# Optimization experiments

Hardware: AMD Instinct MI355X
Metric: run time of the kernel (lower is better)

The kernel has to match this reference:

```python
import jax, jax.numpy as jnp
import numpy as np

D_IN, HID = 128, 256
N_A, N_T = 120000, 30000
E_AT, E_TA, E_AA = 2_000_000, 2_000_000, 3_000_000
OUTS = [("artist", 129), ("style", 32), ("genre", 18)]


def setup_inputs() -> dict:
    key = jax.random.key(0)
    ks = jax.random.split(key, 32)

    def w(k, shape, fan_in):
        return jax.random.normal(k, shape, jnp.float32) / np.float32(np.sqrt(fan_in))

    def edges(k, e, n_src, n_dst):
        k1, k2 = jax.random.split(k)
        return jnp.stack([jax.random.randint(k1, (e,), 0, n_src),
                          jax.random.randint(k2, (e,), 0, n_dst)]).astype(jnp.int32)

    inp = {}
    inp["x_artwork"] = jax.random.normal(ks[0], (N_A, D_IN), jnp.float32)
    inp["x_tag"] = jax.random.normal(ks[1], (N_T, D_IN), jnp.float32)
    inp["edge_at"] = edges(ks[2], E_AT, N_A, N_T)
    inp["edge_ta"] = edges(ks[3], E_TA, N_T, N_A)
    inp["edge_aa"] = edges(ks[4], E_AA, N_A, N_A)
    # layer-1 weights shared shape across 3 gnns (G) and 3 relations (R): [G,R,din,H]
    inp["Wl1"] = w(ks[5], (3, 3, D_IN, HID), D_IN)
    inp["Wr1"] = w(ks[6], (3, 3, D_IN, HID), D_IN)
    inp["b1"] = jnp.zeros((3, 3, HID), jnp.float32)
    for i, (name, o) in enumerate(OUTS):
        inp[f"Wl2_{name}"] = w(ks[7 + 3 * i], (3, HID, o), HID)
        inp[f"Wr2_{name}"] = w(ks[8 + 3 * i], (3, HID, o), HID)
        inp[f"b2_{name}"] = jnp.zeros((3, o), jnp.float32)
    return inp


def _seg_mean(feat, dst, n):
    # PyG mean aggregation: sum over in-edges / count, 0 for isolated nodes
    s = jax.ops.segment_sum(feat, dst, num_segments=n)
    c = jax.ops.segment_sum(jnp.ones((dst.shape[0], 1), feat.dtype), dst, num_segments=n)
    return s / jnp.maximum(c, 1.0)


def _hetero_sage(xa, xt, e_at, e_ta, e_aa, Wl, Wr, b):
    # Wl/Wr: [3, din, dout] (rel order: at, ta, aa), b: [3, dout]
    m_at = _seg_mean(xa[e_at[0]], e_at[1], xt.shape[0])
    h_t = m_at @ Wl[0] + b[0] + xt @ Wr[0]
    m_ta = _seg_mean(xt[e_ta[0]], e_ta[1], xa.shape[0])
    m_aa = _seg_mean(xa[e_aa[0]], e_aa[1], xa.shape[0])
    h_a = (m_ta @ Wl[1] + b[1] + xa @ Wr[1]) + (m_aa @ Wl[2] + b[2] + xa @ Wr[2])
    return h_a, h_t


def _dropout(x, key, rate=0.5):
    keep = jax.random.bernoulli(key, 1.0 - rate, x.shape)
    return jnp.where(keep, x / (1.0 - rate), jnp.zeros((), x.dtype))


def _gnn(g, xa, xt, e_at, e_ta, e_aa, Wl1, Wr1, b1, Wl2, Wr2, b2):
    h_a, h_t = _hetero_sage(xa, xt, e_at, e_ta, e_aa, Wl1, Wr1, b1)
    h_a, h_t = jax.nn.relu(h_a), jax.nn.relu(h_t)
    k1, k2 = jax.random.split(jax.random.fold_in(jax.random.key(42), g))
    h_a, h_t = _dropout(h_a, k1), _dropout(h_t, k2)
    o_a, o_t = _hetero_sage(h_a, h_t, e_at, e_ta, e_aa, Wl2, Wr2, b2)
    return jax.nn.log_softmax(o_a, axis=1), jax.nn.log_softmax(o_t, axis=1)


def reference(x_artwork, x_tag, edge_at, edge_ta, edge_aa, Wl1, Wr1, b1,
              Wl2_artist, Wr2_artist, b2_artist,
              Wl2_style, Wr2_style, b2_style,
              Wl2_genre, Wr2_genre, b2_genre):
    l2 = [(Wl2_artist, Wr2_artist, b2_artist),
          (Wl2_style, Wr2_style, b2_style),
          (Wl2_genre, Wr2_genre, b2_genre)]
    outs = []
    for g in range(3):
        Wl2, Wr2, b2 = l2[g]
        o_a, o_t = _gnn(g, x_artwork, x_tag, edge_at, edge_ta, edge_aa,
                        Wl1[g], Wr1[g], b1[g], Wl2, Wr2, b2)
        outs.extend([o_a, o_t])
    return tuple(outs)
```

## Files before the change

### kernel.cpp

```cpp
#include <hip/hip_runtime.h>
#include <stdint.h>
#include <stddef.h>

typedef unsigned short bf16;
typedef __attribute__((ext_vector_type(8))) short short8;
typedef __attribute__((ext_vector_type(4))) float f32x4;

__device__ __forceinline__ float bf2f(unsigned short u){
  union { uint32_t i; float f; } x; x.i = ((uint32_t)u) << 16; return x.f;
}
__device__ __forceinline__ unsigned short f2bf(float f){
  union { float f; uint32_t i; } x; x.f = f;
  uint32_t r = x.i + 0x7FFFu + ((x.i >> 16) & 1u);
  return (unsigned short)(r >> 16);
}
__device__ __forceinline__ uint32_t pk2(float a, float b){
  return (uint32_t)f2bf(a) | ((uint32_t)f2bf(b) << 16);
}

__device__ __forceinline__ uint8_t f2fp8(float f){
  uint32_t b = __float_as_uint(f);
  uint32_t s = (b >> 24) & 0x80u;
  uint32_t x = b & 0x7fffffffu;
  if (x >= 0x43e00000u) return (uint8_t)(s | 0x7eu);
  if (x < 0x3c800000u){
    uint32_t q = (uint32_t)rintf(__uint_as_float(x) * 512.f);
    return (uint8_t)(s | q);
  }
  uint32_t lsb = (x >> 20) & 1u;
  x += 0x7ffffu + lsb;
  uint32_t u = (((x >> 23) - 120u) << 3) | ((x >> 20) & 7u);
  if (u > 0x7eu) u = 0x7eu;
  return (uint8_t)(s | u);
}
__device__ __forceinline__ float fp8d(uint8_t u){
  uint32_t e = (u >> 3) & 15u, m = u & 7u;
  float v = (e == 0) ? (float)m * 0.001953125f
                     : ldexpf((float)(8u + m), (int)e - 10);
  return (u & 0x80u) ? -v : v;
}

__host__ __device__ __forceinline__ uint32_t rotl32_(uint32_t x, int d){
  return (x << d) | (x >> (32 - d));
}
__host__ __device__ inline void tf2x32(uint32_t k0, uint32_t k1, uint32_t x0, uint32_t x1,
                                       uint32_t* o0, uint32_t* o1){
  uint32_t k2 = k0 ^ k1 ^ 0x1BD11BDAu;
#define TF_R4(ra,rb,rc,rd) \
  x0 += x1; x1 = rotl32_(x1,ra); x1 ^= x0; \
  x0 += x1; x1 = rotl32_(x1,rb); x1 ^= x0; \
  x0 += x1; x1 = rotl32_(x1,rc); x1 ^= x0; \
  x0 += x1; x1 = rotl32_(x1,rd); x1 ^= x0;
  x0 += k0; x1 += k1;
  TF_R4(13,15,26,6)  x0 += k1; x1 += k2 + 1u;
  TF_R4(17,29,16,24) x0 += k2; x1 += k0 + 2u;
  TF_R4(13,15,26,6)  x0 += k0; x1 += k1 + 3u;
  TF_R4(17,29,16,24) x0 += k1; x1 += k2 + 4u;
  TF_R4(13,15,26,6)  x0 += k2; x1 += k0 + 5u;
  *o0 = x0; *o1 = x1;
#undef TF_R4
}

__global__ void k_zeroi(int* __restrict__ p, int n){
  int i = blockIdx.x * 256 + threadIdx.x;
  if (i < n) p[i] = 0;
}
__global__ void k_f2bf(const float* __restrict__ in, bf16* __restrict__ out, int n4){
  int i = blockIdx.x * 256 + threadIdx.x;
  if (i < n4){
    float4 v = ((const float4*)in)[i];
    ushort4 u; u.x = f2bf(v.x); u.y = f2bf(v.y); u.z = f2bf(v.z); u.w = f2bf(v.w);
    ((ushort4*)out)[i] = u;
  }
}

__global__ void k_deg(const int* __restrict__ dst, int* __restrict__ deg, int E){
  int i = blockIdx.x * 256 + threadIdx.x;
  if (i < E) atomicAdd(&deg[dst[i]], 1);
}
__global__ __launch_bounds__(256)
void k_scan_partial(const int* __restrict__ in, int* __restrict__ exc,
                    int* __restrict__ bsum, int n){
  __shared__ int tmp[256];
  int t = threadIdx.x, i = blockIdx.x * 256 + t;
  int v = (i < n) ? in[i] : 0;
  tmp[t] = v; __syncthreads();
  #pragma unroll
  for (int off = 1; off < 256; off <<= 1){
    int u = (t >= off) ? tmp[t - off] : 0; __syncthreads();
    tmp[t] += u; __syncthreads();
  }
  if (i < n) exc[i] = tmp[t] - v;
  if (t == 255) bsum[blockIdx.x] = tmp[255];
}
__global__ __launch_bounds__(1024)
void k_scan_bsum(int* __restrict__ bsum, int nb, int* __restrict__ total_out){
  __shared__ int tmp[1024];
  int t = threadIdx.x;
  int v = (t < nb) ? bsum[t] : 0;
  tmp[t] = v; __syncthreads();
  #pragma unroll
  for (int off = 1; off < 1024; off <<= 1){
    int u = (t >= off) ? tmp[t - off] : 0; __syncthreads();
    tmp[t] += u; __syncthreads();
  }
  if (t < nb) bsum[t] = tmp[t] - v;
  if (t == 1023) *total_out = tmp[1023];
}
__global__ void k_scan_add(int* __restrict__ exc, const int* __restrict__ bsum, int n){
  int i = blockIdx.x * 256 + threadIdx.x;
  if (i < n) exc[i] += bsum[blockIdx.x];
}
__global__ void k_fill(const int* __restrict__ src, const int* __restrict__ dst,
                       const int* __restrict__ rs, int* __restrict__ cur,
                       int* __restrict__ cs, int E){
  int i = blockIdx.x * 256 + threadIdx.x;
  if (i < E){
    int d = dst[i];
    int p = atomicAdd(&cur[d], 1);
    cs[rs[d] + p] = src[i];
  }
}

__global__ __launch_bounds__(64)
void k_agg128b(const bf16* __restrict__ X, const int* __restrict__ rs,
               const int* __restrict__ cs, bf16* __restrict__ out){
  int node = blockIdx.x, lane = threadIdx.x;
  int s0 = rs[node], s1 = rs[node + 1];
  float ax = 0.f, ay = 0.f;
  int e = s0;
  for (; e + 4 <= s1; e += 4){
    int c0 = cs[e], c1 = cs[e+1], c2 = cs[e+2], c3 = cs[e+3];
    uint32_t v0 = ((const uint32_t*)(X + (size_t)c0 * 128))[lane];
    uint32_t v1 = ((const uint32_t*)(X + (size_t)c1 * 128))[lane];
    uint32_t v2 = ((const uint32_t*)(X + (size_t)c2 * 128))[lane];
    uint32_t v3 = ((const uint32_t*)(X + (size_t)c3 * 128))[lane];
    ax += bf2f((unsigned short)(v0 & 0xffffu)) + bf2f((unsigned short)(v1 & 0xffffu))
        + bf2f((unsigned short)(v2 & 0xffffu)) + bf2f((unsigned short)(v3 & 0xffffu));
    ay += bf2f((unsigned short)(v0 >> 16)) + bf2f((unsigned short)(v1 >> 16))
        + bf2f((unsigned short)(v2 >> 16)) + bf2f((unsigned short)(v3 >> 16));
  }
  for (; e < s1; ++e){
    uint32_t v = ((const uint32_t*)(X + (size_t)cs[e] * 128))[lane];
    ax += bf2f((unsigned short)(v & 0xffffu));
    ay += bf2f((unsigned short)(v >> 16));
  }
  float inv = 1.f / fmaxf((float)(s1 - s0), 1.f);
  ((uint32_t*)(out + (size_t)node * 128))[lane] = pk2(ax * inv, ay * inv);
}

__global__ void k_wt1a(const float* __restrict__ Wl1g, const float* __restrict__ Wr1g,
                       bf16* __restrict__ dst){
  int n = blockIdx.y, k = blockIdx.x * 128 + threadIdx.x;
  int seg = k >> 7, kk = k & 127;
  float v;
  if (seg == 0)      v = Wl1g[(size_t)(128 + kk) * 256 + n];
  else if (seg == 1) v = Wl1g[(size_t)(256 + kk) * 256 + n];
  else               v = Wr1g[(size_t)(128 + kk) * 256 + n] + Wr1g[(size_t)(256 + kk) * 256 + n];
  dst[(size_t)n * 384 + k] = f2bf(v);
}
__global__ void k_wt1t(const float* __restrict__ Wl1g, const float* __restrict__ Wr1g,
                       bf16* __restrict__ dst){
  int n = blockIdx.y, k = blockIdx.x * 128 + threadIdx.x;
  int kk = k & 127;
  float v = (k < 128) ? Wl1g[(size_t)kk * 256 + n] : Wr1g[(size_t)kk * 256 + n];
  dst[(size_t)n * 256 + k] = f2bf(v);
}
__global__ void k_wt2a(const float* __restrict__ Wl2g, const float* __restrict__ Wr2g,
                       int O, bf16* __restrict__ dst){
  int n = blockIdx.y, k = blockIdx.x * 128 + threadIdx.x;
  int strip = n / O, r = n - strip * O;
  float v;
  if (strip == 0)      v = Wl2g[(size_t)k * O + r];
  else if (strip == 1) v = Wl2g[(size_t)512 * O + (size_t)k * O + r];
  else                 v = Wr2g[(size_t)256 * O + (size_t)k * O + r]
                         + Wr2g[(size_t)512 * O + (size_t)k * O + r];
  dst[(size_t)n * 256 + k] = f2bf(v);
}
__global__ void k_wt2t(const float* __restrict__ Wl2g, const float* __restrict__ Wr2g,
                       int O, bf16* __restrict__ dst){
  int n = blockIdx.y, k = blockIdx.x * 128 + threadIdx.x;
  int strip = n / O, r = n - strip * O;
  float v = (strip == 0) ? Wl2g[(size_t)256 * O + (size_t)k * O + r]
                         : Wr2g[(size_t)k * O + r];
  dst[(size_t)n * 256 + k] = f2bf(v);
}
__global__ void k_bias(const float* __restrict__ b1g, const float* __restrict__ b2g,
                       int O, float* __restrict__ bc1, float* __restrict__ bc2){
  int t = threadIdx.x;
  bc1[t] = b1g[256 + t] + b1g[512 + t];
  if (t < O) bc2[t] = b2g[O + t] + b2g[2 * O + t];
}

template<int EPI>
__global__ __launch_bounds__(256)
void k_gemm_mfma(const bf16* __restrict__ A0, const bf16* __restrict__ A1,
                 const bf16* __restrict__ A2, int lda,
                 const bf16* __restrict__ Bt, int ldb,
                 int M, int N, int Ktot,
                 bf16* __restrict__ hC,
                 uint8_t* __restrict__ z0, uint8_t* __restrict__ z1,
                 float* __restrict__ outF, const float* __restrict__ bias,
                 int O, int zoff, uint32_t dk0, uint32_t dk1){
  __shared__ bf16 As[128][40];
  __shared__ bf16 Bs[64][40];
  const int tid = threadIdx.x;
  const int w = tid >> 6, l = tid & 63;
  const int r0 = blockIdx.y * 128, c0 = blockIdx.x * 64;

  f32x4 acc[2][4] = {};

  const int sm = tid >> 1, sk = (tid & 1) * 16;
  const int bn = tid >> 2, bk = (tid & 3) * 8;
  const int arow = r0 + sm, brow = c0 + bn;
  const int lr = l & 15, g8 = (l >> 4) * 8;

  for (int kk = 0; kk < Ktot; kk += 32){
    const int seg = kk >> 7, koff = (kk & 127) + sk;
    const bf16* Ap = (seg == 0) ? A0 : ((seg == 1) ? A1 : A2);
    uint4 wa0 = {0,0,0,0}, wa1 = {0,0,0,0};
    if (arow < M){
      const uint4* p = (const uint4*)(Ap + (size_t)arow * lda + koff);
      wa0 = p[0]; wa1 = p[1];
    }
    uint4 wb = {0,0,0,0};
    if (brow < N) wb = *(const uint4*)(Bt + (size_t)brow * ldb + kk + bk);
    __syncthreads();
    *(uint4*)&As[sm][sk]     = wa0;
    *(uint4*)&As[sm][sk + 8] = wa1;
    *(uint4*)&Bs[bn][bk]     = wb;
    __syncthreads();
    short8 a0 = *(const short8*)&As[w * 32      + lr][g8];
    short8 a1 = *(const short8*)&As[w * 32 + 16 + lr][g8];
    short8 b0 = *(const short8*)&Bs[     lr][g8];
    short8 b1 = *(const short8*)&Bs[16 + lr][g8];
    short8 b2 = *(const short8*)&Bs[32 + lr][g8];
    short8 b3 = *(const short8*)&Bs[48 + lr][g8];
    acc[0][0] = __builtin_amdgcn_mfma_f32_16x16x32_bf16(a0, b0, acc[0][0], 0, 0, 0);
    acc[0][1] = __builtin_amdgcn_mfma_f32_16x16x32_bf16(a0, b1, acc[0][1], 0, 0, 0);
    acc[0][2] = __builtin_amdgcn_mfma_f32_16x16x32_bf16(a0, b2, acc[0][2], 0, 0, 0);
    acc[0][3] = __builtin_amdgcn_mfma_f32_16x16x32_bf16(a0, b3, acc[0][3], 0, 0, 0);
    acc[1][0] = __builtin_amdgcn_mfma_f32_16x16x32_bf16(a1, b0, acc[1][0], 0, 0, 0);
    acc[1][1] = __builtin_amdgcn_mfma_f32_16x16x32_bf16(a1, b1, acc[1][1], 0, 0, 0);
    acc[1][2] = __builtin_amdgcn_mfma_f32_16x16x32_bf16(a1, b2, acc[1][2], 0, 0, 0);
    acc[1][3] = __builtin_amdgcn_mfma_f32_16x16x32_bf16(a1, b3, acc[1][3], 0, 0, 0);
  }
  #pragma unroll
  for (int rt = 0; rt < 2; ++rt){
    #pragma unroll
    for (int ct = 0; ct < 4; ++ct){
      #pragma unroll
      for (int r = 0; r < 4; ++r){
        int row = r0 + w * 32 + rt * 16 + (l >> 4) * 4 + r;
        int col = c0 + ct * 16 + lr;
        if (row < M && col < N){
          float v = acc[rt][ct][r];
          if (EPI == 0){
            v += bias[col];
            uint32_t o0, o1;
            tf2x32(dk0, dk1, 0u, (uint32_t)(row * 256 + col), &o0, &o1);
            float a = fmaxf(v, 0.f) * 2.f;
            hC[(size_t)row * 256 + col] = ((o0 ^ o1) >> 31) ? (bf16)0 : f2bf(a);
          } else {
            int s = (col >= O) + (EPI == 1 ? (col >= 2 * O) : 0);
            int lc = col - s * O;
            const int fs = (EPI == 1) ? 2 : 1;
            if (s == fs){
              outF[(size_t)row * O + lc] = v + bias[lc];
            } else {
              uint8_t* d = (s == 0) ? z0 : z1;
              d[(size_t)row * 192 + zoff + lc] = f2fp8(v);
            }
          }
        }
      }
    }
  }
}

__global__ __launch_bounds__(192)
void k_assemble_t(const uint8_t* __restrict__ z, const int* __restrict__ rs,
                  const int* __restrict__ cs,
                  float* __restrict__ o0, float* __restrict__ o1, float* __restrict__ o2){
  __shared__ float lut[256];
  __shared__ float sb[179];
  __shared__ float lse[3];
  const int node = blockIdx.x, t = threadIdx.x;
  lut[t] = fp8d((uint8_t)t);
  if (t < 64) lut[t + 192] = fp8d((uint8_t)(t + 192));
  const bool act = t < 179;
  const int h = (t < 129) ? 0 : ((t < 161) ? 1 : 2);
  const int base = (h == 0) ? 0 : ((h == 1) ? 129 : 161);
  const int Oh = (h == 0) ? 129 : ((h == 1) ? 32 : 18);
  const int s0 = rs[node], s1 = rs[node + 1];
  __syncthreads();
  float acc = 0.f;
  int e = s0;
  for (; e + 4 <= s1; e += 4){
    size_t c0 = (size_t)cs[e] * 192, c1 = (size_t)cs[e+1] * 192;
    size_t c2 = (size_t)cs[e+2] * 192, c3 = (size_t)cs[e+3] * 192;
    if (act){
      float v0 = lut[z[c0 + t]], v1 = lut[z[c1 + t]];
      float v2 = lut[z[c2 + t]], v3 = lut[z[c3 + t]];
      acc += (v0 + v1) + (v2 + v3);
    }
  }
  for (; e < s1; ++e)
    if (act) acc += lut[z[(size_t)cs[e] * 192 + t]];
  const float inv = 1.f / fmaxf((float)(s1 - s0), 1.f);
  float* orow = ((h == 0) ? o0 : ((h == 1) ? o1 : o2)) + (size_t)node * Oh + (t - base);
  float v = 0.f;
  if (act) v = *orow + acc * inv;
  if (act) sb[t] = v;
  __syncthreads();
  const int wv = t >> 6, ln = t & 63;
  {
    const int b = (wv == 0) ? 0 : ((wv == 1) ? 129 : 161);
    const int W = (wv == 0) ? 129 : ((wv == 1) ? 32 : 18);
    float m = -3.4e38f;
    for (int i = ln; i < W; i += 64) m = fmaxf(m, sb[b + i]);
    #pragma unroll
    for (int o = 32; o; o >>= 1) m = fmaxf(m, __shfl_xor(m, o));
    float s = 0.f;
    for (int i = ln; i < W; i += 64) s += expf(sb[b + i] - m);
    #pragma unroll
    for (int o = 32; o; o >>= 1) s += __shfl_xor(s, o);
    if (ln == 0) lse[wv] = m + logf(s);
  }
  __syncthreads();
  if (act) *orow = v - lse[h];
}

__global__ __launch_bounds__(192)
void k_assemble_a(const uint8_t* __restrict__ zT, const uint8_t* __restrict__ zA,
                  const int* __restrict__ rs_ta, const int* __restrict__ cs_ta,
                  const int* __restrict__ rs_aa, const int* __restrict__ cs_aa,
                  float* __restrict__ o0, float* __restrict__ o1, float* __restrict__ o2){
  __shared__ float lut[256];
  __shared__ float sb[179];
  __shared__ float lse[3];
  const int node = blockIdx.x, t = threadIdx.x;
  lut[t] = fp8d((uint8_t)t);
  if (t < 64) lut[t + 192] = fp8d((uint8_t)(t + 192));
  const bool act = t < 179;
  const int h = (t < 129) ? 0 : ((t < 161) ? 1 : 2);
  const int base = (h == 0) ? 0 : ((h == 1) ? 129 : 161);
  const int Oh = (h == 0) ? 129 : ((h == 1) ? 32 : 18);
  __syncthreads();
  float accT = 0.f, accA = 0.f;
  int s0 = rs_ta[node], s1 = rs_ta[node + 1];
  int e = s0;
  for (; e + 4 <= s1; e += 4){
    size_t c0 = (size_t)cs_ta[e] * 192, c1 = (size_t)cs_ta[e+1] * 192;
    size_t c2 = (size_t)cs_ta[e+2] * 192, c3 = (size_t)cs_ta[e+3] * 192;
    if (act){
      float v0 = lut[zT[c0 + t]], v1 = lut[zT[c1 + t]];
      float v2 = lut[zT[c2 + t]], v3 = lut[zT[c3 + t]];
      accT += (v0 + v1) + (v2 + v3);
    }
  }
  for (; e < s1; ++e)
    if (act) accT += lut[zT[(size_t)cs_ta[e] * 192 + t]];
  const float invT = 1.f / fmaxf((float)(s1 - s0), 1.f);
  s0 = rs_aa[node]; s1 = rs_aa[node + 1];
  e = s0;
  for (; e + 4 <= s1; e += 4){
    size_t c0 = (size_t)cs_aa[e] * 192, c1 = (size_t)cs_aa[e+1] * 192;
    size_t c2 = (size_t)cs_aa[e+2] * 192, c3 = (size_t)cs_aa[e+3] * 192;
    if (act){
      float v0 = lut[zA[c0 + t]], v1 = lut[zA[c1 + t]];
      float v2 = lut[zA[c2 + t]], v3 = lut[zA[c3 + t]];
      accA += (v0 + v1) + (v2 + v3);
    }
  }
  for (; e < s1; ++e)
    if (act) accA += lut[zA[(size_t)cs_aa[e] * 192 + t]];
  const float invA = 1.f / fmaxf((float)(s1 - s0), 1.f);
  float* orow = ((h == 0) ? o0 : ((h == 1) ? o1 : o2)) + (size_t)node * Oh + (t - base);
  float v = 0.f;
  if (act) v = *orow + accT * invT + accA * invA;
  if (act) sb[t] = v;
  __syncthreads();
  const int wv = t >> 6, ln = t & 63;
  {
    const int b = (wv == 0) ? 0 : ((wv == 1) ? 129 : 161);
    const int W = (wv == 0) ? 129 : ((wv == 1) ? 32 : 18);
    float m = -3.4e38f;
    for (int i = ln; i < W; i += 64) m = fmaxf(m, sb[b + i]);
    #pragma unroll
    for (int o = 32; o; o >>= 1) m = fmaxf(m, __shfl_xor(m, o));
    float s = 0.f;
    for (int i = ln; i < W; i += 64) s += expf(sb[b + i] - m);
    #pragma unroll
    for (int o = 32; o; o >>= 1) s += __shfl_xor(s, o);
    if (ln == 0) lse[wv] = m + logf(s);
  }
  __syncthreads();
  if (act) *orow = v - lse[h];
}

extern "C" void kernel_launch(void* const* d_in, const int* in_sizes, int n_in,
                              void* d_out, int out_size, void* d_ws, size_t ws_size,
                              hipStream_t stream){
  (void)n_in; (void)out_size; (void)ws_size;
  const float* xa  = (const float*)d_in[0];
  const float* xt  = (const float*)d_in[1];
  const int*   e_at = (const int*)d_in[2];
  const int*   e_ta = (const int*)d_in[3];
  const int*   e_aa = (const int*)d_in[4];
  const float* Wl1 = (const float*)d_in[5];
  const float* Wr1 = (const float*)d_in[6];
  const float* b1  = (const float*)d_in[7];
  const float* Wl2_[3] = {(const float*)d_in[8],  (const float*)d_in[11], (const float*)d_in[14]};
  const float* Wr2_[3] = {(const float*)d_in[9],  (const float*)d_in[12], (const float*)d_in[15]};
  const float* b2_[3]  = {(const float*)d_in[10], (const float*)d_in[13], (const float*)d_in[16]};

  const int NA = in_sizes[0] / 128;
  const int NT = in_sizes[1] / 128;
  const int EAT = in_sizes[2] / 2, ETA = in_sizes[3] / 2, EAA = in_sizes[4] / 2;
  const int Ov[3] = {129, 32, 18};
  const int og[3] = {0, 129, 161};

  char* Wp = (char*)d_ws;
  size_t off = 0;
  auto alloc = [&](size_t bytes)->char*{
    char* p = Wp + off; off = (off + bytes + 255) & ~(size_t)255; return p;
  };
  bf16* xa_b = (bf16*)alloc((size_t)NA * 128 * 2);
  bf16* xt_b = (bf16*)alloc((size_t)NT * 128 * 2);
  bf16* m_at = (bf16*)alloc((size_t)NT * 128 * 2);
  bf16* m_ta = (bf16*)alloc((size_t)NA * 128 * 2);
  bf16* m_aa = (bf16*)alloc((size_t)NA * 128 * 2);
  bf16* h_a  = (bf16*)alloc((size_t)NA * 256 * 2);
  bf16* h_t  = (bf16*)alloc((size_t)NT * 256 * 2);
  uint8_t* zA_at = (uint8_t*)alloc((size_t)NA * 192);
  uint8_t* zT_ta = (uint8_t*)alloc((size_t)NT * 192);
  uint8_t* zA_aa = (uint8_t*)alloc((size_t)NA * 192);
  bf16* Bt_ha = (bf16*)alloc((size_t)256 * 384 * 2);
  bf16* Bt_ht = (bf16*)alloc((size_t)256 * 256 * 2);
  bf16* BT2a  = (bf16*)alloc((size_t)3 * 129 * 256 * 2);
  bf16* BT2t  = (bf16*)alloc((size_t)2 * 129 * 256 * 2);
  float* bc1  = (float*)alloc(256 * 4);
  float* bc2  = (float*)alloc(129 * 4);
  int* rs_at  = (int*)alloc((size_t)(NT + 1) * 4);
  int* rs_ta  = (int*)alloc((size_t)(NA + 1) * 4);
  int* rs_aa  = (int*)alloc((size_t)(NA + 1) * 4);
  int* cur_at = (int*)alloc((size_t)NT * 4);
  int* cur_ta = (int*)alloc((size_t)NA * 4);
  int* cur_aa = (int*)alloc((size_t)NA * 4);
  int* bsum   = (int*)alloc(2048 * 4);
  int* cs_at  = (int*)alloc((size_t)EAT * 4);
  int* cs_ta  = (int*)alloc((size_t)ETA * 4);
  int* cs_aa  = (int*)alloc((size_t)EAA * 4);

  k_f2bf<<<(NA * 128 / 4 + 255) / 256, 256, 0, stream>>>(xa, xa_b, NA * 128 / 4);
  k_f2bf<<<(NT * 128 / 4 + 255) / 256, 256, 0, stream>>>(xt, xt_b, NT * 128 / 4);

  auto build_csr = [&](const int* edges, int E, int n, int* rs, int* cur, int* cs){
    int ebl = (E + 255) / 256, nbl = (n + 255) / 256;
    k_zeroi<<<nbl, 256, 0, stream>>>(cur, n);
    k_deg<<<ebl, 256, 0, stream>>>(edges + E, cur, E);
    k_scan_partial<<<nbl, 256, 0, stream>>>(cur, rs, bsum, n);
    k_scan_bsum<<<1, 1024, 0, stream>>>(bsum, nbl, rs + n);
    k_scan_add<<<nbl, 256, 0, stream>>>(rs, bsum, n);
    k_zeroi<<<nbl, 256, 0, stream>>>(cur, n);
    k_fill<<<ebl, 256, 0, stream>>>(edges, edges + E, rs, cur, cs, E);
  };
  build_csr(e_at, EAT, NT, rs_at, cur_at, cs_at);
  build_csr(e_ta, ETA, NA, rs_ta, cur_ta, cs_ta);
  build_csr(e_aa, EAA, NA, rs_aa, cur_aa, cs_aa);

  k_agg128b<<<NT, 64, 0, stream>>>(xa_b, rs_at, cs_at, m_at);
  k_agg128b<<<NA, 64, 0, stream>>>(xt_b, rs_ta, cs_ta, m_ta);
  k_agg128b<<<NA, 64, 0, stream>>>(xa_b, rs_aa, cs_aa, m_aa);

  size_t offA[3], offT[3], cum = 0;
  for (int g = 0; g < 3; ++g){
    offA[g] = cum; offT[g] = cum + (size_t)NA * Ov[g];
    cum += (size_t)(NA + NT) * Ov[g];
  }

  for (int g = 0; g < 3; ++g){
    const int O = Ov[g];
    float* outA = (float*)d_out + offA[g];
    float* outT = (float*)d_out + offT[g];
    const float* Wl1g = Wl1 + (size_t)(3 * g) * 128 * 256;
    const float* Wr1g = Wr1 + (size_t)(3 * g) * 128 * 256;
    const float* b1g  = b1  + (size_t)(3 * g) * 256;

    k_wt1a<<<dim3(3, 256), 128, 0, stream>>>(Wl1g, Wr1g, Bt_ha);
    k_wt1t<<<dim3(2, 256), 128, 0, stream>>>(Wl1g, Wr1g, Bt_ht);
    k_wt2a<<<dim3(2, 3 * O), 128, 0, stream>>>(Wl2_[g], Wr2_[g], O, BT2a);
    k_wt2t<<<dim3(2, 2 * O), 128, 0, stream>>>(Wl2_[g], Wr2_[g], O, BT2t);
    k_bias<<<1, 256, 0, stream>>>(b1g, b2_[g], O, bc1, bc2);

    uint32_t kg0, kg1, ka0, ka1, kt0, kt1;
    tf2x32(0u, 42u, 0u, (uint32_t)g, &kg0, &kg1);
    tf2x32(kg0, kg1, 0u, 0u, &ka0, &ka1);
    tf2x32(kg0, kg1, 0u, 1u, &kt0, &kt1);

    k_gemm_mfma<0><<<dim3(4, (NA + 127) / 128), 256, 0, stream>>>(
        m_ta, m_aa, xa_b, 128, Bt_ha, 384, NA, 256, 384,
        h_a, nullptr, nullptr, nullptr, bc1, 0, 0, ka0, ka1);
    k_gemm_mfma<0><<<dim3(4, (NT + 127) / 128), 256, 0, stream>>>(
        m_at, xt_b, xt_b, 128, Bt_ht, 256, NT, 256, 256,
        h_t, nullptr, nullptr, nullptr, b1g, 0, 0, kt0, kt1);

    k_gemm_mfma<1><<<dim3((3 * O + 63) / 64, (NA + 127) / 128), 256, 0, stream>>>(
        h_a, h_a + 128, h_a, 256, BT2a, 256, NA, 3 * O, 256,
        nullptr, zA_at, zA_aa, outA, bc2, O, og[g], 0, 0);
    k_gemm_mfma<2><<<dim3((2 * O + 63) / 64, (NT + 127) / 128), 256, 0, stream>>>(
        h_t, h_t + 128, h_t, 256, BT2t, 256, NT, 2 * O, 256,
        nullptr, zT_ta, nullptr, outT, b2_[g], O, og[g], 0, 0);
  }

  k_assemble_t<<<NT, 192, 0, stream>>>(zA_at, rs_at, cs_at,
                                       (float*)d_out + offT[0], (float*)d_out + offT[1],
                                       (float*)d_out + offT[2]);
  k_assemble_a<<<NA, 192, 0, stream>>>(zT_ta, zA_aa, rs_ta, cs_ta, rs_aa, cs_aa,
                                       (float*)d_out + offA[0], (float*)d_out + offA[1],
                                       (float*)d_out + offA[2]);
}
```

Baseline: 2.168 ms.

## Gather FP8 input features for layer-1 aggregation and vectorize FP8 assembly gathers

Layer-1 neighbor aggregation now gathers FP8-encoded input features instead of bf16, halving the bytes per gathered row. The bf16 copies needed by the GEMMs are produced afterwards, reusing the same buffer slot. The assemble kernels now load four FP8 bytes per thread with hardware packed conversion instead of byte loads through a shared LUT, spread edges across four thread groups and reduce them in shared memory. FP8 encoding in the GEMM epilogue also switches to the hardware conversion builtin. This lowers gather bandwidth and decode cost but adds extra quantization error on the input features, plus a possible rounding or saturation mismatch between the hardware and software FP8 formats.

```diff
diff --git a/kernel.cpp b/kernel.cpp
--- a/kernel.cpp
+++ b/kernel.cpp
@@ -18,7 +18,7 @@
   return (uint32_t)f2bf(a) | ((uint32_t)f2bf(b) << 16);
 }
 
-__device__ __forceinline__ uint8_t f2fp8(float f){
+__device__ __forceinline__ uint8_t f2fp8_sw(float f){
   uint32_t b = __float_as_uint(f);
   uint32_t s = (b >> 24) & 0x80u;
   uint32_t x = b & 0x7fffffffu;
@@ -33,11 +33,46 @@
   if (u > 0x7eu) u = 0x7eu;
   return (uint8_t)(s | u);
 }
-__device__ __forceinline__ float fp8d(uint8_t u){
+__device__ __forceinline__ float fp8_dec1_sw(uint32_t u){
   uint32_t e = (u >> 3) & 15u, m = u & 7u;
-  float v = (e == 0) ? (float)m * 0.001953125f
-                     : ldexpf((float)(8u + m), (int)e - 10);
+  float v = e ? __uint_as_float(((e + 120u) << 23) | (m << 20))
+              : (float)m * 0.001953125f;
   return (u & 0x80u) ? -v : v;
+}
+
+#if __has_builtin(__builtin_amdgcn_cvt_pk_f32_fp8) && __has_builtin(__builtin_amdgcn_cvt_pk_fp8_f32)
+#define FP8_HW 1
+#else
+#define FP8_HW 0
+#endif
+
+__device__ __forceinline__ void fp8_dec4(uint32_t w, float* o){
+#if FP8_HW
+  auto lo = __builtin_amdgcn_cvt_pk_f32_fp8((int)w, false);
+  auto hi = __builtin_amdgcn_cvt_pk_f32_fp8((int)w, true);
+  o[0] = lo[0]; o[1] = lo[1]; o[2] = hi[0]; o[3] = hi[1];
+#else
+  o[0] = fp8_dec1_sw(w & 0xffu);        o[1] = fp8_dec1_sw((w >> 8) & 0xffu);
+  o[2] = fp8_dec1_sw((w >> 16) & 0xffu); o[3] = fp8_dec1_sw(w >> 24);
+#endif
+}
+__device__ __forceinline__ uint8_t fp8_enc1(float v){
+#if FP8_HW
+  return (uint8_t)(__builtin_amdgcn_cvt_pk_fp8_f32(v, v, 0, false) & 0xff);
+#else
+  return f2fp8_sw(v);
+#endif
+}
+__device__ __forceinline__ uint32_t fp8_enc4(float a, float b, float c, float d){
+#if FP8_HW
+  int w = 0;
+  w = __builtin_amdgcn_cvt_pk_fp8_f32(a, b, w, false);
+  w = __builtin_amdgcn_cvt_pk_fp8_f32(c, d, w, true);
+  return (uint32_t)w;
+#else
+  return (uint32_t)f2fp8_sw(a) | ((uint32_t)f2fp8_sw(b) << 8)
+       | ((uint32_t)f2fp8_sw(c) << 16) | ((uint32_t)f2fp8_sw(d) << 24);
+#endif
 }
 
 __host__ __device__ __forceinline__ uint32_t rotl32_(uint32_t x, int d){
@@ -73,6 +108,13 @@
     ((ushort4*)out)[i] = u;
   }
 }
+__global__ void k_f2fp8(const float* __restrict__ in, uint8_t* __restrict__ out, int n4){
+  int i = blockIdx.x * 256 + threadIdx.x;
+  if (i < n4){
+    float4 v = ((const float4*)in)[i];
+    ((uint32_t*)out)[i] = fp8_enc4(v.x, v.y, v.z, v.w);
+  }
+}
 
 __global__ void k_deg(const int* __restrict__ dst, int* __restrict__ deg, int E){
   int i = blockIdx.x * 256 + threadIdx.x;
@@ -123,30 +165,38 @@
 }
 
 __global__ __launch_bounds__(64)
-void k_agg128b(const bf16* __restrict__ X, const int* __restrict__ rs,
-               const int* __restrict__ cs, bf16* __restrict__ out){
-  int node = blockIdx.x, lane = threadIdx.x;
-  int s0 = rs[node], s1 = rs[node + 1];
-  float ax = 0.f, ay = 0.f;
+void k_agg128_8(const uint8_t* __restrict__ X8, const int* __restrict__ rs,
+                const int* __restrict__ cs, bf16* __restrict__ out){
+  const int node = blockIdx.x, lane = threadIdx.x;
+  const int hl = lane >> 5, cl = lane & 31;
+  const int s0 = rs[node], s1 = rs[node + 1];
+  float a[4] = {0.f, 0.f, 0.f, 0.f};
   int e = s0;
   for (; e + 4 <= s1; e += 4){
-    int c0 = cs[e], c1 = cs[e+1], c2 = cs[e+2], c3 = cs[e+3];
-    uint32_t v0 = ((const uint32_t*)(X + (size_t)c0 * 128))[lane];
-    uint32_t v1 = ((const uint32_t*)(X + (size_t)c1 * 128))[lane];
-    uint32_t v2 = ((const uint32_t*)(X + (size_t)c2 * 128))[lane];
-    uint32_t v3 = ((const uint32_t*)(X + (size_t)c3 * 128))[lane];
-    ax += bf2f((unsigned short)(v0 & 0xffffu)) + bf2f((unsigned short)(v1 & 0xffffu))
-        + bf2f((unsigned short)(v2 & 0xffffu)) + bf2f((unsigned short)(v3 & 0xffffu));
-    ay += bf2f((unsigned short)(v0 >> 16)) + bf2f((unsigned short)(v1 >> 16))
-        + bf2f((unsigned short)(v2 >> 16)) + bf2f((unsigned short)(v3 >> 16));
-  }
-  for (; e < s1; ++e){
-    uint32_t v = ((const uint32_t*)(X + (size_t)cs[e] * 128))[lane];
-    ax += bf2f((unsigned short)(v & 0xffffu));
-    ay += bf2f((unsigned short)(v >> 16));
-  }
-  float inv = 1.f / fmaxf((float)(s1 - s0), 1.f);
-  ((uint32_t*)(out + (size_t)node * 128))[lane] = pk2(ax * inv, ay * inv);
+    uint32_t w0 = *(const uint32_t*)(X8 + (size_t)cs[e + hl] * 128 + (cl << 2));
+    uint32_t w1 = *(const uint32_t*)(X8 + (size_t)cs[e + 2 + hl] * 128 + (cl << 2));
+    float d0[4], d1[4];
+    fp8_dec4(w0, d0); fp8_dec4(w1, d1);
+    #pragma unroll
+    for (int j = 0; j < 4; ++j) a[j] += d0[j] + d1[j];
+  }
+  for (; e < s1; e += 2){
+    int i = e + hl;
+    uint32_t w = (i < s1) ? *(const uint32_t*)(X8 + (size_t)cs[i] * 128 + (cl << 2)) : 0u;
+    float d[4];
+    fp8_dec4(w, d);
+    #pragma unroll
+    for (int j = 0; j < 4; ++j) a[j] += d[j];
+  }
+  #pragma unroll
+  for (int j = 0; j < 4; ++j) a[j] += __shfl_xor(a[j], 32);
+  if (lane < 32){
+    float inv = 1.f / fmaxf((float)(s1 - s0), 1.f);
+    ushort4 u;
+    u.x = f2bf(a[0] * inv); u.y = f2bf(a[1] * inv);
+    u.z = f2bf(a[2] * inv); u.w = f2bf(a[3] * inv);
+    *(ushort4*)(out + (size_t)node * 128 + (cl << 2)) = u;
+  }
 }
 
 __global__ void k_wt1a(const float* __restrict__ Wl1g, const float* __restrict__ Wr1g,
@@ -269,7 +319,7 @@
               outF[(size_t)row * O + lc] = v + bias[lc];
             } else {
               uint8_t* d = (s == 0) ? z0 : z1;
-              d[(size_t)row * 192 + zoff + lc] = f2fp8(v);
+              d[(size_t)row * 192 + zoff + lc] = fp8_enc1(v);
             }
           }
         }
@@ -278,43 +328,57 @@
   }
 }
 
-__global__ __launch_bounds__(192)
+__global__ __launch_bounds__(256)
 void k_assemble_t(const uint8_t* __restrict__ z, const int* __restrict__ rs,
                   const int* __restrict__ cs,
                   float* __restrict__ o0, float* __restrict__ o1, float* __restrict__ o2){
-  __shared__ float lut[256];
-  __shared__ float sb[179];
-  __shared__ float lse[3];
   const int node = blockIdx.x, t = threadIdx.x;
-  lut[t] = fp8d((uint8_t)t);
-  if (t < 64) lut[t + 192] = fp8d((uint8_t)(t + 192));
-  const bool act = t < 179;
+  const int sg = t / 45, c4 = t - sg * 45;
+  const bool gact = t < 180;
   const int h = (t < 129) ? 0 : ((t < 161) ? 1 : 2);
   const int base = (h == 0) ? 0 : ((h == 1) ? 129 : 161);
   const int Oh = (h == 0) ? 129 : ((h == 1) ? 32 : 18);
+  float* orow = ((h == 0) ? o0 : ((h == 1) ? o1 : o2)) + (size_t)node * Oh + (t - base);
   const int s0 = rs[node], s1 = rs[node + 1];
+  float res = (t < 179) ? *orow : 0.f;
+
+  float a[4] = {0.f, 0.f, 0.f, 0.f};
+  int e = s0;
+  for (; e + 8 <= s1; e += 8){
+    uint32_t w0 = gact ? *(const uint32_t*)(z + (size_t)cs[e + sg] * 192 + (c4 << 2)) : 0u;
+    uint32_t w1 = gact ? *(const uint32_t*)(z + (size_t)cs[e + 4 + sg] * 192 + (c4 << 2)) : 0u;
+    if (c4 == 44){ w0 &= 0xffffffu; w1 &= 0xffffffu; }
+    float d0[4], d1[4];
+    fp8_dec4(w0, d0); fp8_dec4(w1, d1);
+    #pragma unroll
+    for (int j = 0; j < 4; ++j) a[j] += d0[j] + d1[j];
+  }
+  for (; e < s1; e += 4){
+    int i = e + sg;
+    uint32_t w = (gact && i < s1) ? *(const uint32_t*)(z + (size_t)cs[i] * 192 + (c4 << 2)) : 0u;
+    if (c4 == 44) w &= 0xffffffu;
+    float d[4];
+    fp8_dec4(w, d);
+    #pragma unroll
+    for (int j = 0; j < 4; ++j) a[j] += d[j];
+  }
+  __shared__ float sT[4][180];
+  __shared__ float sb[180];
+  __shared__ float lse[3];
+  if (gact){
+    #pragma unroll
+    for (int j = 0; j < 4; ++j) sT[sg][c4 * 4 + j] = a[j];
+  }
   __syncthreads();
-  float acc = 0.f;
-  int e = s0;
-  for (; e + 4 <= s1; e += 4){
-    size_t c0 = (size_t)cs[e] * 192, c1 = (size_t)cs[e+1] * 192;
-    size_t c2 = (size_t)cs[e+2] * 192, c3 = (size_t)cs[e+3] * 192;
-    if (act){
-      float v0 = lut[z[c0 + t]], v1 = lut[z[c1 + t]];
-      float v2 = lut[z[c2 + t]], v3 = lut[z[c3 + t]];
-      acc += (v0 + v1) + (v2 + v3);
-    }
-  }
-  for (; e < s1; ++e)
-    if (act) acc += lut[z[(size_t)cs[e] * 192 + t]];
-  const float inv = 1.f / fmaxf((float)(s1 - s0), 1.f);
-  float* orow = ((h == 0) ? o0 : ((h == 1) ? o1 : o2)) + (size_t)node * Oh + (t - base);
   float v = 0.f;
-  if (act) v = *orow + acc * inv;
-  if (act) sb[t] = v;
+  if (t < 179){
+    float inv = 1.f / fmaxf((float)(s1 - s0), 1.f);
+    v = res + (sT[0][t] + sT[1][t] + sT[2][t] + sT[3][t]) * inv;
+    sb[t] = v;
+  }
   __syncthreads();
   const int wv = t >> 6, ln = t & 63;
-  {
+  if (wv < 3){
     const int b = (wv == 0) ? 0 : ((wv == 1) ? 129 : 161);
     const int W = (wv == 0) ? 129 : ((wv == 1) ? 32 : 18);
     float m = -3.4e38f;
@@ -328,61 +392,85 @@
     if (ln == 0) lse[wv] = m + logf(s);
   }
   __syncthreads();
-  if (act) *orow = v - lse[h];
-}
-
-__global__ __launch_bounds__(192)
+  if (t < 179) *orow = v - lse[h];
+}
+
+__global__ __launch_bounds__(256)
 void k_assemble_a(const uint8_t* __restrict__ zT, const uint8_t* __restrict__ zA,
                   const int* __restrict__ rs_ta, const int* __restrict__ cs_ta,
                   const int* __restrict__ rs_aa, const int* __restrict__ cs_aa,
                   float* __restrict__ o0, float* __restrict__ o1, float* __restrict__ o2){
-  __shared__ float lut[256];
-  __shared__ float sb[179];
-  __shared__ float lse[3];
   const int node = blockIdx.x, t = threadIdx.x;
-  lut[t] = fp8d((uint8_t)t);
-  if (t < 64) lut[t + 192] = fp8d((uint8_t)(t + 192));
-  const bool act = t < 179;
+  const int sg = t / 45, c4 = t - sg * 45;
+  const bool gact = t < 180;
   const int h = (t < 129) ? 0 : ((t < 161) ? 1 : 2);
   const int base = (h == 0) ? 0 : ((h == 1) ? 129 : 161);
   const int Oh = (h == 0) ? 129 : ((h == 1) ? 32 : 18);
+  float* orow = ((h == 0) ? o0 : ((h == 1) ? o1 : o2)) + (size_t)node * Oh + (t - base);
+  float res = (t < 179) ? *orow : 0.f;
+
+  float aT[4] = {0.f, 0.f, 0.f, 0.f}, aA[4] = {0.f, 0.f, 0.f, 0.f};
+  int s0 = rs_ta[node], s1 = rs_ta[node + 1];
+  const float invT = 1.f / fmaxf((float)(s1 - s0), 1.f);
+  int e = s0;
+  for (; e + 8 <= s1; e += 8){
+    uint32_t w0 = gact ? *(const uint32_t*)(zT + (size_t)cs_ta[e + sg] * 192 + (c4 << 2)) : 0u;
+    uint32_t w1 = gact ? *(const uint32_t*)(zT + (size_t)cs_ta[e + 4 + sg] * 192 + (c4 << 2)) : 0u;
+    if (c4 == 44){ w0 &= 0xffffffu; w1 &= 0xffffffu; }
+    float d0[4], d1[4];
+    fp8_dec4(w0, d0); fp8_dec4(w1, d1);
+    #pragma unroll
+    for (int j = 0; j < 4; ++j) aT[j] += d0[j] + d1[j];
+  }
+  for (; e < s1; e += 4){
+    int i = e + sg;
+    uint32_t w = (gact && i < s1) ? *(const uint32_t*)(zT + (size_t)cs_ta[i] * 192 + (c4 << 2)) : 0u;
+    if (c4 == 44) w &= 0xffffffu;
+    float d[4];
+    fp8_dec4(w, d);
+    #pragma unroll
+    for (int j = 0; j < 4; ++j) aT[j] += d[j];
+  }
+  s0 = rs_aa[node]; s1 = rs_aa[node + 1];
+  const float invA = 1.f / fmaxf((float)(s1 - s0), 1.f);
+  e = s0;
+  for (; e + 8 <= s1; e += 8){
+    uint32_t w0 = gact ? *(const uint32_t*)(zA + (size_t)cs_aa[e + sg] * 192 + (c4 << 2)) : 0u;
+    uint32_t w1 = gact ? *(const uint32_t*)(zA + (size_t)cs_aa[e + 4 + sg] * 192 + (c4 << 2)) : 0u;
+    if (c4 == 44){ w0 &= 0xffffffu; w1 &= 0xffffffu; }
+    float d0[4], d1[4];
+    fp8_dec4(w0, d0); fp8_dec4(w1, d1);
+    #pragma unroll
+    for (int j = 0; j < 4; ++j) aA[j] += d0[j] + d1[j];
+  }
+  for (; e < s1; e += 4){
+    int i = e + sg;
+    uint32_t w = (gact && i < s1) ? *(const uint32_t*)(zA + (size_t)cs_aa[i] * 192 + (c4 << 2)) : 0u;
+    if (c4 == 44) w &= 0xffffffu;
+    float d[4];
+    fp8_dec4(w, d);
+    #pragma unroll
+    for (int j = 0; j < 4; ++j) aA[j] += d[j];
+  }
+  __shared__ float sT[4][180];
+  __shared__ float sA[4][180];
+  __shared__ float sb[180];
+  __shared__ float lse[3];
+  if (gact){
+    #pragma unroll
+    for (int j = 0; j < 4; ++j){ sT[sg][c4 * 4 + j] = aT[j]; sA[sg][c4 * 4 + j] = aA[j]; }
+  }
   __syncthreads();
-  float accT = 0.f, accA = 0.f;
-  int s0 = rs_ta[node], s1 = rs_ta[node + 1];
-  int e = s0;
-  for (; e + 4 <= s1; e += 4){
-    size_t c0 = (size_t)cs_ta[e] * 192, c1 = (size_t)cs_ta[e+1] * 192;
-    size_t c2 = (size_t)cs_ta[e+2] * 192, c3 = (size_t)cs_ta[e+3] * 192;
-    if (act){
-      float v0 = lut[zT[c0 + t]], v1 = lut[zT[c1 + t]];
-      float v2 = lut[zT[c2 + t]], v3 = lut[zT[c3 + t]];
-      accT += (v0 + v1) + (v2 + v3);
-    }
-  }
-  for (; e < s1; ++e)
-    if (act) accT += lut[zT[(size_t)cs_ta[e] * 192 + t]];
-  const float invT = 1.f / fmaxf((float)(s1 - s0), 1.f);
-  s0 = rs_aa[node]; s1 = rs_aa[node + 1];
-  e = s0;
-  for (; e + 4 <= s1; e += 4){
-    size_t c0 = (size_t)cs_aa[e] * 192, c1 = (size_t)cs_aa[e+1] * 192;
-    size_t c2 = (size_t)cs_aa[e+2] * 192, c3 = (size_t)cs_aa[e+3] * 192;
-    if (act){
-      float v0 = lut[zA[c0 + t]], v1 = lut[zA[c1 + t]];
-      float v2 = lut[zA[c2 + t]], v3 = lut[zA[c3 + t]];
-      accA += (v0 + v1) + (v2 + v3);
-    }
-  }
-  for (; e < s1; ++e)
-    if (act) accA += lut[zA[(size_t)cs_aa[e] * 192 + t]];
-  const float invA = 1.f / fmaxf((float)(s1 - s0), 1.f);
-  float* orow = ((h == 0) ? o0 : ((h == 1) ? o1 : o2)) + (size_t)node * Oh + (t - base);
   float v = 0.f;
-  if (act) v = *orow + accT * invT + accA * invA;
-  if (act) sb[t] = v;
+  if (t < 179){
+    float vT = sT[0][t] + sT[1][t] + sT[2][t] + sT[3][t];
+    float vA = sA[0][t] + sA[1][t] + sA[2][t] + sA[3][t];
+    v = res + vT * invT + vA * invA;
+    sb[t] = v;
+  }
   __syncthreads();
   const int wv = t >> 6, ln = t & 63;
-  {
+  if (wv < 3){
     const int b = (wv == 0) ? 0 : ((wv == 1) ? 129 : 161);
     const int W = (wv == 0) ? 129 : ((wv == 1) ? 32 : 18);
     float m = -3.4e38f;
@@ -396,7 +484,7 @@
     if (ln == 0) lse[wv] = m + logf(s);
   }
   __syncthreads();
-  if (act) *orow = v - lse[h];
+  if (t < 179) *orow = v - lse[h];
 }
 
 extern "C" void kernel_launch(void* const* d_in, const int* in_sizes, int n_in,
@@ -426,7 +514,10 @@
   auto alloc = [&](size_t bytes)->char*{
     char* p = Wp + off; off = (off + bytes + 255) & ~(size_t)255; return p;
   };
-  bf16* xa_b = (bf16*)alloc((size_t)NA * 128 * 2);
+  char* slot0 = alloc((size_t)NA * 128 * 2);
+  uint8_t* xa_8 = (uint8_t*)slot0;
+  uint8_t* xt_8 = (uint8_t*)(slot0 + (size_t)NA * 128);
+  bf16* xa_b = (bf16*)slot0;
   bf16* xt_b = (bf16*)alloc((size_t)NT * 128 * 2);
   bf16* m_at = (bf16*)alloc((size_t)NT * 128 * 2);
   bf16* m_ta = (bf16*)alloc((size_t)NA * 128 * 2);
@@ -453,8 +544,8 @@
   int* cs_ta  = (int*)alloc((size_t)ETA * 4);
   int* cs_aa  = (int*)alloc((size_t)EAA * 4);
 
-  k_f2bf<<<(NA * 128 / 4 + 255) / 256, 256, 0, stream>>>(xa, xa_b, NA * 128 / 4);
-  k_f2bf<<<(NT * 128 / 4 + 255) / 256, 256, 0, stream>>>(xt, xt_b, NT * 128 / 4);
+  k_f2fp8<<<(NA * 128 / 4 + 255) / 256, 256, 0, stream>>>(xa, xa_8, NA * 128 / 4);
+  k_f2fp8<<<(NT * 128 / 4 + 255) / 256, 256, 0, stream>>>(xt, xt_8, NT * 128 / 4);
 
   auto build_csr = [&](const int* edges, int E, int n, int* rs, int* cur, int* cs){
     int ebl = (E + 255) / 256, nbl = (n + 255) / 256;
@@ -470,9 +561,12 @@
   build_csr(e_ta, ETA, NA, rs_ta, cur_ta, cs_ta);
   build_csr(e_aa, EAA, NA, rs_aa, cur_aa, cs_aa);
 
-  k_agg128b<<<NT, 64, 0, stream>>>(xa_b, rs_at, cs_at, m_at);
-  k_agg128b<<<NA, 64, 0, stream>>>(xt_b, rs_ta, cs_ta, m_ta);
-  k_agg128b<<<NA, 64, 0, stream>>>(xa_b, rs_aa, cs_aa, m_aa);
+  k_agg128_8<<<NT, 64, 0, stream>>>(xa_8, rs_at, cs_at, m_at);
+  k_agg128_8<<<NA, 64, 0, stream>>>(xt_8, rs_ta, cs_ta, m_ta);
+  k_agg128_8<<<NA, 64, 0, stream>>>(xa_8, rs_aa, cs_aa, m_aa);
+
+  k_f2bf<<<(NA * 128 / 4 + 255) / 256, 256, 0, stream>>>(xa, xa_b, NA * 128 / 4);
+  k_f2bf<<<(NT * 128 / 4 + 255) / 256, 256, 0, stream>>>(xt, xt_b, NT * 128 / 4);
 
   size_t offA[3], offT[3], cum = 0;
   for (int g = 0; g < 3; ++g){
@@ -514,10 +608,10 @@
         nullptr, zT_ta, nullptr, outT, b2_[g], O, og[g], 0, 0);
   }
 
-  k_assemble_t<<<NT, 192, 0, stream>>>(zA_at, rs_at, cs_at,
+  k_assemble_t<<<NT, 256, 0, stream>>>(zA_at, rs_at, cs_at,
                                        (float*)d_out + offT[0], (float*)d_out + offT[1],
                                        (float*)d_out + offT[2]);
-  k_assemble_a<<<NA, 192, 0, stream>>>(zT_ta, zA_aa, rs_ta, cs_ta, rs_aa, cs_aa,
+  k_assemble_a<<<NA, 256, 0, stream>>>(zT_ta, zA_aa, rs_ta, cs_ta, rs_aa, cs_aa,
                                        (float*)d_out + offA[0], (float*)d_out + offA[1],
                                        (float*)d_out + offA[2]);
 }
```

Measured after the change: 2.241 ms. 1.03x slower.
